# Kernel tuning notes

Hardware: AMD Instinct MI355X
Metric: run time of the kernel (lower is better)

## Reference

```python
import jax, jax.numpy as jnp
import numpy as np

HEAD_DIM = 64
SCALE = 1.0 / np.sqrt(HEAD_DIM)  # canonical 1/sqrt(d_k)


def setup_inputs() -> dict:
    key = jax.random.key(0)
    kq, kk, kv = jax.random.split(key, 3)
    B, Lq, Lk, D = 16, 2048, 2048, HEAD_DIM
    q = jax.random.normal(kq, (B, Lq, D), dtype=jnp.float32)
    k = jax.random.normal(kk, (B, Lk, D), dtype=jnp.float32)
    v = jax.random.normal(kv, (B, Lk, D), dtype=jnp.float32)
    return {"q": q, "k": k, "v": v}


def reference(q, k, v):
    # scores: [B, Lq, Lk] = q @ k^T, scaled by 1/sqrt(d)
    scores = jnp.einsum("bqd,bkd->bqk", q, k) * SCALE
    # softmax over the key axis (dim=2), numerically stable
    attention = jax.nn.softmax(scores, axis=2)
    # dropout prob = 0.0 -> identity
    context = jnp.einsum("bqk,bkd->bqd", attention, v)  # [B, Lq, D]
    return (context, attention)
```

## Files before the change

kernel.cpp:

```cpp
#include <hip/hip_runtime.h>
#include <hip/hip_bf16.h>

#define B_   16
#define LQ   2048
#define LK   2048
#define HD   64
#define QT   32
#define KT   64
#define NKT  (LK / KT)
#define SCALE 0.125f

typedef __attribute__((ext_vector_type(8))) short bf16x8;
typedef __attribute__((ext_vector_type(4))) float f32x4;
typedef __attribute__((ext_vector_type(4))) unsigned short us4;

__device__ __forceinline__ unsigned short f2bf(float x) {
    union { float f; unsigned u; } v; v.f = x;
    unsigned r = v.u + 0x7FFFu + ((v.u >> 16) & 1u);
    return (unsigned short)(r >> 16);
}

__device__ __forceinline__ int swz(int row, int col) {
    return (row << 6) + (col ^ ((row & 7) << 3));
}

__global__ __launch_bounds__(256) void sdpa_kernel(
    const float* __restrict__ qg, const float* __restrict__ kg,
    const float* __restrict__ vg, float* __restrict__ ctx,
    float* __restrict__ att)
{
    __shared__ unsigned short Qb[QT * HD];
    __shared__ unsigned short Kb[KT * HD];
    __shared__ unsigned short Vt[HD * KT];
    __shared__ unsigned short Pb[QT * KT];
    __shared__ float redl[4][QT];
    __shared__ float invl[QT];

    const int tid  = threadIdx.x;
    const int wave = tid >> 6;
    const int lane = tid & 63;
    const int g    = lane >> 4;
    const int c    = lane & 15;

    const int b  = blockIdx.x / (LQ / QT);
    const int qt = blockIdx.x % (LQ / QT);

    const float* qp = qg + (b * LQ + qt * QT) * HD;
    const float* kp = kg + b * LK * HD;
    const float* vp = vg + b * LK * HD;
    float* ctxp = ctx + (b * LQ + qt * QT) * HD;
    float* attp = att + ((size_t)(b * LQ + qt * QT)) * LK;

    #pragma unroll
    for (int i = 0; i < 2; ++i) {
        int id  = tid + i * 256;
        int row = id >> 4;
        int c4  = (id & 15) << 2;
        float4 t = *reinterpret_cast<const float4*>(qp + row * HD + c4);
        us4 p = { f2bf(t.x), f2bf(t.y), f2bf(t.z), f2bf(t.w) };
        *reinterpret_cast<us4*>(&Qb[swz(row, c4)]) = p;
    }
    __syncthreads();

    bf16x8 aQ[2][2];
    #pragma unroll
    for (int m = 0; m < 2; ++m)
        #pragma unroll
        for (int h = 0; h < 2; ++h)
            aQ[m][h] = *reinterpret_cast<const bf16x8*>(&Qb[swz(m * 16 + c, h * 32 + g * 8)]);

    float lsum[2][4] = {{0.f,0.f,0.f,0.f},{0.f,0.f,0.f,0.f}};
    for (int t = 0; t < NKT; ++t) {
        __syncthreads();
        #pragma unroll
        for (int i = 0; i < 4; ++i) {
            int id  = tid + i * 256;
            int row = id >> 4;
            int c4  = (id & 15) << 2;
            float4 tk = *reinterpret_cast<const float4*>(kp + (t * KT + row) * HD + c4);
            us4 p = { f2bf(tk.x), f2bf(tk.y), f2bf(tk.z), f2bf(tk.w) };
            *reinterpret_cast<us4*>(&Kb[swz(row, c4)]) = p;
        }
        __syncthreads();
        bf16x8 bK0 = *reinterpret_cast<const bf16x8*>(&Kb[swz(wave * 16 + c, g * 8)]);
        bf16x8 bK1 = *reinterpret_cast<const bf16x8*>(&Kb[swz(wave * 16 + c, 32 + g * 8)]);
        #pragma unroll
        for (int m = 0; m < 2; ++m) {
            f32x4 acc = {0.f, 0.f, 0.f, 0.f};
            acc = __builtin_amdgcn_mfma_f32_16x16x32_bf16(aQ[m][0], bK0, acc, 0, 0, 0);
            acc = __builtin_amdgcn_mfma_f32_16x16x32_bf16(aQ[m][1], bK1, acc, 0, 0, 0);
            #pragma unroll
            for (int r = 0; r < 4; ++r)
                lsum[m][r] += __expf(acc[r] * SCALE);
        }
    }

    #pragma unroll
    for (int m = 0; m < 2; ++m)
        #pragma unroll
        for (int r = 0; r < 4; ++r) {
            float s = lsum[m][r];
            s += __shfl_xor(s, 1, 64);
            s += __shfl_xor(s, 2, 64);
            s += __shfl_xor(s, 4, 64);
            s += __shfl_xor(s, 8, 64);
            lsum[m][r] = s;
        }
    if (c == 0) {
        #pragma unroll
        for (int m = 0; m < 2; ++m)
            #pragma unroll
            for (int r = 0; r < 4; ++r)
                redl[wave][m * 16 + g * 4 + r] = lsum[m][r];
    }
    __syncthreads();
    if (tid < QT) {
        float s = redl[0][tid] + redl[1][tid] + redl[2][tid] + redl[3][tid];
        invl[tid] = 1.0f / s;
    }
    __syncthreads();

    float il[2][4];
    #pragma unroll
    for (int m = 0; m < 2; ++m)
        #pragma unroll
        for (int r = 0; r < 4; ++r)
            il[m][r] = invl[m * 16 + g * 4 + r];

    f32x4 cacc[2];
    cacc[0] = (f32x4){0.f, 0.f, 0.f, 0.f};
    cacc[1] = (f32x4){0.f, 0.f, 0.f, 0.f};

    for (int t = 0; t < NKT; ++t) {
        __syncthreads();
        #pragma unroll
        for (int i = 0; i < 4; ++i) {
            int id  = tid + i * 256;
            int row = id >> 4;
            int c4  = (id & 15) << 2;
            float4 tk = *reinterpret_cast<const float4*>(kp + (t * KT + row) * HD + c4);
            us4 pk = { f2bf(tk.x), f2bf(tk.y), f2bf(tk.z), f2bf(tk.w) };
            *reinterpret_cast<us4*>(&Kb[swz(row, c4)]) = pk;
            float4 tv = *reinterpret_cast<const float4*>(vp + (t * KT + row) * HD + c4);
            Vt[swz(c4 + 0, row)] = f2bf(tv.x);
            Vt[swz(c4 + 1, row)] = f2bf(tv.y);
            Vt[swz(c4 + 2, row)] = f2bf(tv.z);
            Vt[swz(c4 + 3, row)] = f2bf(tv.w);
        }
        __syncthreads();
        bf16x8 bK0 = *reinterpret_cast<const bf16x8*>(&Kb[swz(wave * 16 + c, g * 8)]);
        bf16x8 bK1 = *reinterpret_cast<const bf16x8*>(&Kb[swz(wave * 16 + c, 32 + g * 8)]);
        float pv[2][4];
        #pragma unroll
        for (int m = 0; m < 2; ++m) {
            f32x4 acc = {0.f, 0.f, 0.f, 0.f};
            acc = __builtin_amdgcn_mfma_f32_16x16x32_bf16(aQ[m][0], bK0, acc, 0, 0, 0);
            acc = __builtin_amdgcn_mfma_f32_16x16x32_bf16(aQ[m][1], bK1, acc, 0, 0, 0);
            #pragma unroll
            for (int r = 0; r < 4; ++r)
                pv[m][r] = __expf(acc[r] * SCALE) * il[m][r];
        }
        #pragma unroll
        for (int m = 0; m < 2; ++m)
            #pragma unroll
            for (int r = 0; r < 4; ++r) {
                int row = m * 16 + g * 4 + r;
                int col = wave * 16 + c;
                attp[(size_t)row * LK + t * KT + col] = pv[m][r];
                Pb[swz(row, col)] = f2bf(pv[m][r]);
            }
        __syncthreads();
        bf16x8 bV0 = *reinterpret_cast<const bf16x8*>(&Vt[swz(wave * 16 + c, g * 8)]);
        bf16x8 bV1 = *reinterpret_cast<const bf16x8*>(&Vt[swz(wave * 16 + c, 32 + g * 8)]);
        #pragma unroll
        for (int m = 0; m < 2; ++m) {
            bf16x8 aP0 = *reinterpret_cast<const bf16x8*>(&Pb[swz(m * 16 + c, g * 8)]);
            bf16x8 aP1 = *reinterpret_cast<const bf16x8*>(&Pb[swz(m * 16 + c, 32 + g * 8)]);
            cacc[m] = __builtin_amdgcn_mfma_f32_16x16x32_bf16(aP0, bV0, cacc[m], 0, 0, 0);
            cacc[m] = __builtin_amdgcn_mfma_f32_16x16x32_bf16(aP1, bV1, cacc[m], 0, 0, 0);
        }
    }

    #pragma unroll
    for (int m = 0; m < 2; ++m)
        #pragma unroll
        for (int r = 0; r < 4; ++r)
            ctxp[(m * 16 + g * 4 + r) * HD + wave * 16 + c] = cacc[m][r];
}

extern "C" void kernel_launch(void* const* d_in, const int* in_sizes, int n_in,
                              void* d_out, int out_size, void* d_ws, size_t ws_size,
                              hipStream_t stream) {
    const float* q = (const float*)d_in[0];
    const float* k = (const float*)d_in[1];
    const float* v = (const float*)d_in[2];
    float* ctx = (float*)d_out;
    float* att = ctx + (size_t)B_ * LQ * HD;
    dim3 grid(B_ * (LQ / QT));
    sdpa_kernel<<<grid, dim3(256), 0, stream>>>(q, k, v, ctx, att);
}
```

Baseline: 207.4 us.

## Load K/V fragments directly into registers with prefetch, drop shared staging

Each wave now loads its own K and V fragments straight from global memory into registers and converts them to bf16, prefetching the next tile while computing the current one. This removes the shared-memory staging of Q, K and V and most block barriers. P is double-buffered in shared memory so only one barrier per tile remains. The change also uses exp2f with a folded log2e scale and hardware bf16 conversion intrinsics. V is now read with strided scalar loads and K tiles are fetched redundantly across waves, which may raise global or L2 traffic.

```diff
diff --git a/kernel.cpp b/kernel.cpp
--- a/kernel.cpp
+++ b/kernel.cpp
@@ -8,31 +8,44 @@
 #define QT   32
 #define KT   64
 #define NKT  (LK / KT)
-#define SCALE 0.125f
+#define EC   0.1803368801f
 
 typedef __attribute__((ext_vector_type(8))) short bf16x8;
 typedef __attribute__((ext_vector_type(4))) float f32x4;
-typedef __attribute__((ext_vector_type(4))) unsigned short us4;
-
-__device__ __forceinline__ unsigned short f2bf(float x) {
-    union { float f; unsigned u; } v; v.f = x;
-    unsigned r = v.u + 0x7FFFu + ((v.u >> 16) & 1u);
-    return (unsigned short)(r >> 16);
-}
+
+#define MFMA __builtin_amdgcn_mfma_f32_16x16x32_bf16
 
 __device__ __forceinline__ int swz(int row, int col) {
     return (row << 6) + (col ^ ((row & 7) << 3));
 }
 
-__global__ __launch_bounds__(256) void sdpa_kernel(
+__device__ __forceinline__ bf16x8 cvt8(float4 a, float4 b) {
+    union { bf16x8 v; __hip_bfloat162 h[4]; } u;
+    u.h[0] = __float22bfloat162_rn(make_float2(a.x, a.y));
+    u.h[1] = __float22bfloat162_rn(make_float2(a.z, a.w));
+    u.h[2] = __float22bfloat162_rn(make_float2(b.x, b.y));
+    u.h[3] = __float22bfloat162_rn(make_float2(b.z, b.w));
+    return u.v;
+}
+__device__ __forceinline__ bf16x8 cvt8s(const float* v) {
+    union { bf16x8 r; __hip_bfloat162 h[4]; } u;
+    #pragma unroll
+    for (int i = 0; i < 4; ++i)
+        u.h[i] = __float22bfloat162_rn(make_float2(v[2 * i], v[2 * i + 1]));
+    return u.r;
+}
+__device__ __forceinline__ unsigned short bfbits(float x) {
+    union { __hip_bfloat16 h; unsigned short s; } u;
+    u.h = __float2bfloat16(x);
+    return u.s;
+}
+
+__global__ __launch_bounds__(256, 4) void sdpa_kernel(
     const float* __restrict__ qg, const float* __restrict__ kg,
     const float* __restrict__ vg, float* __restrict__ ctx,
     float* __restrict__ att)
 {
-    __shared__ unsigned short Qb[QT * HD];
-    __shared__ unsigned short Kb[KT * HD];
-    __shared__ unsigned short Vt[HD * KT];
-    __shared__ unsigned short Pb[QT * KT];
+    __shared__ unsigned short Pb[2][QT * KT];
     __shared__ float redl[4][QT];
     __shared__ float invl[QT];
 
@@ -45,53 +58,49 @@
     const int b  = blockIdx.x / (LQ / QT);
     const int qt = blockIdx.x % (LQ / QT);
 
-    const float* qp = qg + (b * LQ + qt * QT) * HD;
-    const float* kp = kg + b * LK * HD;
-    const float* vp = vg + b * LK * HD;
-    float* ctxp = ctx + (b * LQ + qt * QT) * HD;
-    float* attp = att + ((size_t)(b * LQ + qt * QT)) * LK;
-
-    #pragma unroll
-    for (int i = 0; i < 2; ++i) {
-        int id  = tid + i * 256;
-        int row = id >> 4;
-        int c4  = (id & 15) << 2;
-        float4 t = *reinterpret_cast<const float4*>(qp + row * HD + c4);
-        us4 p = { f2bf(t.x), f2bf(t.y), f2bf(t.z), f2bf(t.w) };
-        *reinterpret_cast<us4*>(&Qb[swz(row, c4)]) = p;
-    }
-    __syncthreads();
+    const float* qp = qg + (size_t)(b * LQ + qt * QT) * HD;
+    const float* kp = kg + (size_t)b * LK * HD;
+    const float* vp = vg + (size_t)b * LK * HD;
+    float* ctxp = ctx + (size_t)(b * LQ + qt * QT) * HD;
+    float* attp = att + (size_t)(b * LQ + qt * QT) * LK;
 
     bf16x8 aQ[2][2];
     #pragma unroll
     for (int m = 0; m < 2; ++m)
         #pragma unroll
-        for (int h = 0; h < 2; ++h)
-            aQ[m][h] = *reinterpret_cast<const bf16x8*>(&Qb[swz(m * 16 + c, h * 32 + g * 8)]);
+        for (int h = 0; h < 2; ++h) {
+            const float* p = qp + (m * 16 + c) * HD + h * 32 + g * 8;
+            aQ[m][h] = cvt8(*reinterpret_cast<const float4*>(p),
+                            *reinterpret_cast<const float4*>(p + 4));
+        }
+
+    const float* kl = kp + (wave * 16 + c) * HD + g * 8;
+    const float* vl = vp + (g * 8) * HD + wave * 16 + c;
 
     float lsum[2][4] = {{0.f,0.f,0.f,0.f},{0.f,0.f,0.f,0.f}};
+    float4 ka0 = *reinterpret_cast<const float4*>(kl);
+    float4 ka1 = *reinterpret_cast<const float4*>(kl + 4);
+    float4 kb0 = *reinterpret_cast<const float4*>(kl + 32);
+    float4 kb1 = *reinterpret_cast<const float4*>(kl + 36);
+    #pragma unroll 1
     for (int t = 0; t < NKT; ++t) {
-        __syncthreads();
-        #pragma unroll
-        for (int i = 0; i < 4; ++i) {
-            int id  = tid + i * 256;
-            int row = id >> 4;
-            int c4  = (id & 15) << 2;
-            float4 tk = *reinterpret_cast<const float4*>(kp + (t * KT + row) * HD + c4);
-            us4 p = { f2bf(tk.x), f2bf(tk.y), f2bf(tk.z), f2bf(tk.w) };
-            *reinterpret_cast<us4*>(&Kb[swz(row, c4)]) = p;
-        }
-        __syncthreads();
-        bf16x8 bK0 = *reinterpret_cast<const bf16x8*>(&Kb[swz(wave * 16 + c, g * 8)]);
-        bf16x8 bK1 = *reinterpret_cast<const bf16x8*>(&Kb[swz(wave * 16 + c, 32 + g * 8)]);
+        bf16x8 bK0 = cvt8(ka0, ka1);
+        bf16x8 bK1 = cvt8(kb0, kb1);
+        if (t + 1 < NKT) {
+            const float* n = kl + (size_t)(t + 1) * KT * HD;
+            ka0 = *reinterpret_cast<const float4*>(n);
+            ka1 = *reinterpret_cast<const float4*>(n + 4);
+            kb0 = *reinterpret_cast<const float4*>(n + 32);
+            kb1 = *reinterpret_cast<const float4*>(n + 36);
+        }
         #pragma unroll
         for (int m = 0; m < 2; ++m) {
             f32x4 acc = {0.f, 0.f, 0.f, 0.f};
-            acc = __builtin_amdgcn_mfma_f32_16x16x32_bf16(aQ[m][0], bK0, acc, 0, 0, 0);
-            acc = __builtin_amdgcn_mfma_f32_16x16x32_bf16(aQ[m][1], bK1, acc, 0, 0, 0);
+            acc = MFMA(aQ[m][0], bK0, acc, 0, 0, 0);
+            acc = MFMA(aQ[m][1], bK1, acc, 0, 0, 0);
             #pragma unroll
             for (int r = 0; r < 4; ++r)
-                lsum[m][r] += __expf(acc[r] * SCALE);
+                lsum[m][r] += exp2f(acc[r] * EC);
         }
     }
 
@@ -131,54 +140,70 @@
     cacc[0] = (f32x4){0.f, 0.f, 0.f, 0.f};
     cacc[1] = (f32x4){0.f, 0.f, 0.f, 0.f};
 
+    ka0 = *reinterpret_cast<const float4*>(kl);
+    ka1 = *reinterpret_cast<const float4*>(kl + 4);
+    kb0 = *reinterpret_cast<const float4*>(kl + 32);
+    kb1 = *reinterpret_cast<const float4*>(kl + 36);
+    float va[8], vb[8];
+    #pragma unroll
+    for (int j = 0; j < 8; ++j) {
+        va[j] = vl[(size_t)j * HD];
+        vb[j] = vl[(size_t)(32 + j) * HD];
+    }
+
+    int buf = 0;
+    #pragma unroll 1
     for (int t = 0; t < NKT; ++t) {
-        __syncthreads();
-        #pragma unroll
-        for (int i = 0; i < 4; ++i) {
-            int id  = tid + i * 256;
-            int row = id >> 4;
-            int c4  = (id & 15) << 2;
-            float4 tk = *reinterpret_cast<const float4*>(kp + (t * KT + row) * HD + c4);
-            us4 pk = { f2bf(tk.x), f2bf(tk.y), f2bf(tk.z), f2bf(tk.w) };
-            *reinterpret_cast<us4*>(&Kb[swz(row, c4)]) = pk;
-            float4 tv = *reinterpret_cast<const float4*>(vp + (t * KT + row) * HD + c4);
-            Vt[swz(c4 + 0, row)] = f2bf(tv.x);
-            Vt[swz(c4 + 1, row)] = f2bf(tv.y);
-            Vt[swz(c4 + 2, row)] = f2bf(tv.z);
-            Vt[swz(c4 + 3, row)] = f2bf(tv.w);
-        }
-        __syncthreads();
-        bf16x8 bK0 = *reinterpret_cast<const bf16x8*>(&Kb[swz(wave * 16 + c, g * 8)]);
-        bf16x8 bK1 = *reinterpret_cast<const bf16x8*>(&Kb[swz(wave * 16 + c, 32 + g * 8)]);
-        float pv[2][4];
+        bf16x8 bK0 = cvt8(ka0, ka1);
+        bf16x8 bK1 = cvt8(kb0, kb1);
+        bf16x8 bV0 = cvt8s(va);
+        bf16x8 bV1 = cvt8s(vb);
+
+        float pr[2][4];
         #pragma unroll
         for (int m = 0; m < 2; ++m) {
             f32x4 acc = {0.f, 0.f, 0.f, 0.f};
-            acc = __builtin_amdgcn_mfma_f32_16x16x32_bf16(aQ[m][0], bK0, acc, 0, 0, 0);
-            acc = __builtin_amdgcn_mfma_f32_16x16x32_bf16(aQ[m][1], bK1, acc, 0, 0, 0);
+            acc = MFMA(aQ[m][0], bK0, acc, 0, 0, 0);
+            acc = MFMA(aQ[m][1], bK1, acc, 0, 0, 0);
             #pragma unroll
             for (int r = 0; r < 4; ++r)
-                pv[m][r] = __expf(acc[r] * SCALE) * il[m][r];
-        }
+                pr[m][r] = exp2f(acc[r] * EC) * il[m][r];
+        }
+
+        if (t + 1 < NKT) {
+            const float* n = kl + (size_t)(t + 1) * KT * HD;
+            ka0 = *reinterpret_cast<const float4*>(n);
+            ka1 = *reinterpret_cast<const float4*>(n + 4);
+            kb0 = *reinterpret_cast<const float4*>(n + 32);
+            kb1 = *reinterpret_cast<const float4*>(n + 36);
+            const float* nv = vl + (size_t)(t + 1) * KT * HD;
+            #pragma unroll
+            for (int j = 0; j < 8; ++j) {
+                va[j] = nv[(size_t)j * HD];
+                vb[j] = nv[(size_t)(32 + j) * HD];
+            }
+        }
+
         #pragma unroll
         for (int m = 0; m < 2; ++m)
             #pragma unroll
             for (int r = 0; r < 4; ++r) {
                 int row = m * 16 + g * 4 + r;
                 int col = wave * 16 + c;
-                attp[(size_t)row * LK + t * KT + col] = pv[m][r];
-                Pb[swz(row, col)] = f2bf(pv[m][r]);
+                attp[(size_t)row * LK + t * KT + col] = pr[m][r];
+                Pb[buf][swz(row, col)] = bfbits(pr[m][r]);
             }
-        __syncthreads();
-        bf16x8 bV0 = *reinterpret_cast<const bf16x8*>(&Vt[swz(wave * 16 + c, g * 8)]);
-        bf16x8 bV1 = *reinterpret_cast<const bf16x8*>(&Vt[swz(wave * 16 + c, 32 + g * 8)]);
+
+        asm volatile("s_waitcnt lgkmcnt(0)\n\ts_barrier" ::: "memory");
+
         #pragma unroll
         for (int m = 0; m < 2; ++m) {
-            bf16x8 aP0 = *reinterpret_cast<const bf16x8*>(&Pb[swz(m * 16 + c, g * 8)]);
-            bf16x8 aP1 = *reinterpret_cast<const bf16x8*>(&Pb[swz(m * 16 + c, 32 + g * 8)]);
-            cacc[m] = __builtin_amdgcn_mfma_f32_16x16x32_bf16(aP0, bV0, cacc[m], 0, 0, 0);
-            cacc[m] = __builtin_amdgcn_mfma_f32_16x16x32_bf16(aP1, bV1, cacc[m], 0, 0, 0);
-        }
+            bf16x8 aP0 = *reinterpret_cast<const bf16x8*>(&Pb[buf][swz(m * 16 + c, g * 8)]);
+            bf16x8 aP1 = *reinterpret_cast<const bf16x8*>(&Pb[buf][swz(m * 16 + c, 32 + g * 8)]);
+            cacc[m] = MFMA(aP0, bV0, cacc[m], 0, 0, 0);
+            cacc[m] = MFMA(aP1, bV1, cacc[m], 0, 0, 0);
+        }
+        buf ^= 1;
     }
 
     #pragma unroll
```

After: 208.6 us. No clear change (+0.6%).
